# Optimization experiments

Hardware: AMD Instinct MI355X
Metric: run time of the kernel (lower is better)

The kernel has to match this reference:

```python
import jax, jax.numpy as jnp
import numpy as np

B, S, H = 1024, 512, 768
D1, D2 = 128, 1


def setup_inputs() -> dict:
    key = jax.random.key(0)
    k_feat, k_start, k_len, k_w1, k_w2 = jax.random.split(key, 5)
    features_extract = jax.random.normal(k_feat, (B, S, H), dtype=jnp.float32)
    start_token_idx = jax.random.randint(k_start, (B,), 1, 200, dtype=jnp.int64)
    span_len = jax.random.randint(k_len, (B,), 1, 65, dtype=jnp.int64)
    end_token_idx = start_token_idx + span_len  # guaranteed start < end <= 264 < S
    W1 = jax.random.normal(k_w1, (2 * H, D1), dtype=jnp.float32) * (1.0 / np.sqrt(2 * H))
    b1 = jnp.zeros((D1,), dtype=jnp.float32)
    W2 = jax.random.normal(k_w2, (D1, D2), dtype=jnp.float32) * (1.0 / np.sqrt(D1))
    b2 = jnp.zeros((D2,), dtype=jnp.float32)
    return {
        "features_extract": features_extract,
        "start_token_idx": start_token_idx,
        "end_token_idx": end_token_idx,
        "W1": W1, "b1": b1, "W2": W2, "b2": b2,
    }


def reference(features_extract, start_token_idx, end_token_idx, W1, b1, W2, b2):
    # CLS feature: token 0 of each example -> [B, 1, H]
    features_cls = features_extract[:, 0, :][:, None, :]

    # Ragged span mean-pool (vectorized replacement for the per-example loop):
    # mask[b, s] = start[b] <= s < end[b]
    pos = jnp.arange(features_extract.shape[1])  # [S]
    mask = (pos[None, :] >= start_token_idx[:, None]) & (pos[None, :] < end_token_idx[:, None])
    maskf = mask.astype(features_extract.dtype)  # [B, S]
    span_sum = jnp.einsum('bsh,bs->bh', features_extract, maskf)
    span_len = (end_token_idx - start_token_idx).astype(features_extract.dtype)  # >= 1
    features_crc = (span_sum / span_len[:, None])[:, None, :]  # [B, 1, H]

    # Concat + MLP head (dropout layers are identity in eval)
    features = jnp.concatenate([features_cls, features_crc], axis=2)  # [B, 1, 2H]
    h = jax.nn.relu(jnp.einsum('bid,dk->bik', features, W1) + b1)
    out = jax.nn.sigmoid(jnp.einsum('bik,ko->bio', h, W2) + b2)  # [B, 1, 1]
    return out
```

## Files before the change

kernel.cpp:

```cpp
#include <hip/hip_runtime.h>
#include <math.h>

constexpr int Bn = 1024;
constexpr int S  = 512;
constexpr int H  = 768;
constexpr int D1 = 128;
constexpr int HV = H / 4;
constexpr int NH = 512;


__global__ __launch_bounds__(256) void fused_pool_clshead(
    const float* __restrict__ feat, const int* __restrict__ start,
    const int* __restrict__ endp, float* __restrict__ gp,
    const float* __restrict__ W1, float* __restrict__ P) {
  __shared__ float g[4][384];
  __shared__ float part[2][4][D1];

  const int t = threadIdx.x;

  if (blockIdx.x < NH) {
    const int c = blockIdx.x & 1;
    const int e0 = (blockIdx.x >> 1) * 4;
    const int dglob0 = c * 384;

    for (int i = t; i < 384; i += 256) {
      const int e = i / 96;
      const int j = i % 96;
      float4 v = *reinterpret_cast<const float4*>(
          feat + (size_t)(e0 + e) * S * H + dglob0 + j * 4);
      reinterpret_cast<float4*>(&g[e][0])[j] = v;
    }
    __syncthreads();

    const int k = t & (D1 - 1);
    const int sub = t >> 7;
    const int gofs = sub * 192;
    const float* Wc = W1 + (size_t)(dglob0 + gofs) * D1 + k;

    float a0 = 0.f, a1 = 0.f, a2 = 0.f, a3 = 0.f;
    #pragma unroll 4
    for (int d = 0; d < 192; d += 4) {
      float w0 = Wc[(size_t)(d + 0) * D1];
      float w1 = Wc[(size_t)(d + 1) * D1];
      float w2 = Wc[(size_t)(d + 2) * D1];
      float w3 = Wc[(size_t)(d + 3) * D1];
      float4 g0 = *reinterpret_cast<const float4*>(&g[0][gofs + d]);
      float4 g1 = *reinterpret_cast<const float4*>(&g[1][gofs + d]);
      float4 g2 = *reinterpret_cast<const float4*>(&g[2][gofs + d]);
      float4 g3 = *reinterpret_cast<const float4*>(&g[3][gofs + d]);
      a0 += g0.x * w0 + g0.y * w1 + g0.z * w2 + g0.w * w3;
      a1 += g1.x * w0 + g1.y * w1 + g1.z * w2 + g1.w * w3;
      a2 += g2.x * w0 + g2.y * w1 + g2.z * w2 + g2.w * w3;
      a3 += g3.x * w0 + g3.y * w1 + g3.z * w2 + g3.w * w3;
    }
    part[sub][0][k] = a0;
    part[sub][1][k] = a1;
    part[sub][2][k] = a2;
    part[sub][3][k] = a3;
    __syncthreads();

    if (t < D1) {
      #pragma unroll
      for (int e = 0; e < 4; ++e) {
        P[((size_t)c * Bn + (e0 + e)) * D1 + t] = part[0][e][t] + part[1][e][t];
      }
    }
    return;
  }

  if (t >= 192) return;
  const int bb = blockIdx.x - NH;
  const int b = bb >> 1;
  const int p = bb & 1;
  const float4* base = reinterpret_cast<const float4*>(feat) + (size_t)b * (S * HV);

  const int s0 = start[b];
  const int s1 = endp[b];
  float4 a0{0,0,0,0}, a1{0,0,0,0}, a2{0,0,0,0}, a3{0,0,0,0};
  int s = s0 + p;
  for (; s + 6 < s1; s += 8) {
    float4 v0 = base[(size_t)(s    ) * HV + t];
    float4 v1 = base[(size_t)(s + 2) * HV + t];
    float4 v2 = base[(size_t)(s + 4) * HV + t];
    float4 v3 = base[(size_t)(s + 6) * HV + t];
    a0.x += v0.x; a0.y += v0.y; a0.z += v0.z; a0.w += v0.w;
    a1.x += v1.x; a1.y += v1.y; a1.z += v1.z; a1.w += v1.w;
    a2.x += v2.x; a2.y += v2.y; a2.z += v2.z; a2.w += v2.w;
    a3.x += v3.x; a3.y += v3.y; a3.z += v3.z; a3.w += v3.w;
  }
  for (; s < s1; s += 2) {
    float4 v = base[(size_t)s * HV + t];
    a0.x += v.x; a0.y += v.y; a0.z += v.z; a0.w += v.w;
  }
  const float inv = 1.0f / (float)(s1 - s0);
  float4 r;
  r.x = ((a0.x + a1.x) + (a2.x + a3.x)) * inv;
  r.y = ((a0.y + a1.y) + (a2.y + a3.y)) * inv;
  r.z = ((a0.z + a1.z) + (a2.z + a3.z)) * inv;
  r.w = ((a0.w + a1.w) + (a2.w + a3.w)) * inv;
  reinterpret_cast<float4*>(gp)[((size_t)p * Bn + b) * HV + t] = r;
}

__global__ __launch_bounds__(256) void crc_head_finalize(
    const float* __restrict__ gp, const float* __restrict__ W1,
    const float* __restrict__ P, const float* __restrict__ b1,
    const float* __restrict__ W2, const float* __restrict__ b2,
    float* __restrict__ out) {
  __shared__ float g[4][768];
  __shared__ float part[2][4][D1];

  const int t = threadIdx.x;
  const int e0 = blockIdx.x * 4;

  for (int i = t; i < 768; i += 256) {
    const int e = i / 192;
    const int j = i % 192;
    const float* b0 = gp + (size_t)(e0 + e) * H;
    float4 u0 = reinterpret_cast<const float4*>(b0)[j];
    float4 u1 = reinterpret_cast<const float4*>(b0 + (size_t)Bn * H)[j];
    float4 v;
    v.x = u0.x + u1.x; v.y = u0.y + u1.y;
    v.z = u0.z + u1.z; v.w = u0.w + u1.w;
    reinterpret_cast<float4*>(&g[e][0])[j] = v;
  }
  __syncthreads();

  const int k = t & (D1 - 1);
  const int sub = t >> 7;
  const int gofs = sub * 384;
  const float* Wc = W1 + (size_t)(H + gofs) * D1 + k;

  float a0 = 0.f, a1 = 0.f, a2 = 0.f, a3 = 0.f;
  #pragma unroll 4
  for (int d = 0; d < 384; d += 4) {
    float w0 = Wc[(size_t)(d + 0) * D1];
    float w1 = Wc[(size_t)(d + 1) * D1];
    float w2 = Wc[(size_t)(d + 2) * D1];
    float w3 = Wc[(size_t)(d + 3) * D1];
    float4 g0 = *reinterpret_cast<const float4*>(&g[0][gofs + d]);
    float4 g1 = *reinterpret_cast<const float4*>(&g[1][gofs + d]);
    float4 g2 = *reinterpret_cast<const float4*>(&g[2][gofs + d]);
    float4 g3 = *reinterpret_cast<const float4*>(&g[3][gofs + d]);
    a0 += g0.x * w0 + g0.y * w1 + g0.z * w2 + g0.w * w3;
    a1 += g1.x * w0 + g1.y * w1 + g1.z * w2 + g1.w * w3;
    a2 += g2.x * w0 + g2.y * w1 + g2.z * w2 + g2.w * w3;
    a3 += g3.x * w0 + g3.y * w1 + g3.z * w2 + g3.w * w3;
  }
  part[sub][0][k] = a0;
  part[sub][1][k] = a1;
  part[sub][2][k] = a2;
  part[sub][3][k] = a3;
  __syncthreads();

  {
    const int w = t >> 6, l = t & 63;
    const int e = e0 + w;
    const int k0 = l, k1 = l + 64;
    float h0 = b1[k0] + part[0][w][k0] + part[1][w][k0]
             + P[((size_t)0 * Bn + e) * D1 + k0]
             + P[((size_t)1 * Bn + e) * D1 + k0];
    float h1 = b1[k1] + part[0][w][k1] + part[1][w][k1]
             + P[((size_t)0 * Bn + e) * D1 + k1]
             + P[((size_t)1 * Bn + e) * D1 + k1];
    h0 = fmaxf(h0, 0.f); h1 = fmaxf(h1, 0.f);
    float v = h0 * W2[k0] + h1 * W2[k1];
    #pragma unroll
    for (int off = 32; off > 0; off >>= 1) v += __shfl_down(v, off);
    if (l == 0) out[e] = 1.0f / (1.0f + expf(-(v + b2[0])));
  }
}

extern "C" void kernel_launch(void* const* d_in, const int* in_sizes, int n_in,
                              void* d_out, int out_size, void* d_ws, size_t ws_size,
                              hipStream_t stream) {
  const float* feat = (const float*)d_in[0];
  const int* start  = (const int*)d_in[1];
  const int* endp   = (const int*)d_in[2];
  const float* W1   = (const float*)d_in[3];
  const float* b1   = (const float*)d_in[4];
  const float* W2   = (const float*)d_in[5];
  const float* b2   = (const float*)d_in[6];
  float* out = (float*)d_out;

  float* wsf = (float*)d_ws;
  float* gp  = wsf;
  float* P   = gp + (size_t)2 * Bn * H;

  hipLaunchKernelGGL(fused_pool_clshead, dim3(NH + Bn * 2), dim3(256), 0,
                     stream, feat, start, endp, gp, W1, P);
  hipLaunchKernelGGL(crc_head_finalize, dim3(Bn / 4), dim3(256), 0, stream,
                     gp, W1, P, b1, W2, b2, out);
}
```

Measured before the change: 36.93 us.

## Merge pool and head kernels into one launch with atomic flag dataflow

Result: slower. 143.5 us (+288.7%).

```diff
diff --git a/kernel.cpp b/kernel.cpp
--- a/kernel.cpp
+++ b/kernel.cpp
@@ -6,21 +6,78 @@
 constexpr int H  = 768;
 constexpr int D1 = 128;
 constexpr int HV = H / 4;
-constexpr int NH = 512;
-
-
-__global__ __launch_bounds__(256) void fused_pool_clshead(
+
+constexpr int NPOOL = Bn * 2;
+constexpr int NCLS  = 512;
+constexpr int NCRC  = 512;
+constexpr int NFIN  = Bn / 4;
+
+
+__device__ __forceinline__ void release_add(unsigned* f) {
+  __hip_atomic_fetch_add(f, 1u, __ATOMIC_RELEASE, __HIP_MEMORY_SCOPE_AGENT);
+}
+__device__ __forceinline__ void acquire_spin(const unsigned* f, unsigned need) {
+  while (__hip_atomic_load(f, __ATOMIC_ACQUIRE, __HIP_MEMORY_SCOPE_AGENT) < need) {
+    __builtin_amdgcn_s_sleep(8);
+  }
+}
+
+__global__ __launch_bounds__(256) void mega(
     const float* __restrict__ feat, const int* __restrict__ start,
-    const int* __restrict__ endp, float* __restrict__ gp,
-    const float* __restrict__ W1, float* __restrict__ P) {
+    const int* __restrict__ endp, const float* __restrict__ W1,
+    const float* __restrict__ b1, const float* __restrict__ W2,
+    const float* __restrict__ b2, unsigned* __restrict__ flag1,
+    unsigned* __restrict__ flag2, float* __restrict__ gp,
+    float* __restrict__ P, float* __restrict__ out) {
   __shared__ float g[4][384];
   __shared__ float part[2][4][D1];
 
   const int t = threadIdx.x;
-
-  if (blockIdx.x < NH) {
-    const int c = blockIdx.x & 1;
-    const int e0 = (blockIdx.x >> 1) * 4;
+  const unsigned bid = blockIdx.x;
+
+  if (bid < NPOOL) {
+    const int b = bid >> 1;
+    const int p = bid & 1;
+    const int eg = b >> 2;
+    if (t < 192) {
+      const float4* base =
+          reinterpret_cast<const float4*>(feat) + (size_t)b * (S * HV);
+      const int s0 = start[b];
+      const int s1 = endp[b];
+      float4 a0{0,0,0,0}, a1{0,0,0,0}, a2{0,0,0,0}, a3{0,0,0,0};
+      int s = s0 + p;
+      for (; s + 6 < s1; s += 8) {
+        float4 v0 = base[(size_t)(s    ) * HV + t];
+        float4 v1 = base[(size_t)(s + 2) * HV + t];
+        float4 v2 = base[(size_t)(s + 4) * HV + t];
+        float4 v3 = base[(size_t)(s + 6) * HV + t];
+        a0.x += v0.x; a0.y += v0.y; a0.z += v0.z; a0.w += v0.w;
+        a1.x += v1.x; a1.y += v1.y; a1.z += v1.z; a1.w += v1.w;
+        a2.x += v2.x; a2.y += v2.y; a2.z += v2.z; a2.w += v2.w;
+        a3.x += v3.x; a3.y += v3.y; a3.z += v3.z; a3.w += v3.w;
+      }
+      for (; s < s1; s += 2) {
+        float4 v = base[(size_t)s * HV + t];
+        a0.x += v.x; a0.y += v.y; a0.z += v.z; a0.w += v.w;
+      }
+      const float inv = 1.0f / (float)(s1 - s0);
+      float4 r;
+      r.x = ((a0.x + a1.x) + (a2.x + a3.x)) * inv;
+      r.y = ((a0.y + a1.y) + (a2.y + a3.y)) * inv;
+      r.z = ((a0.z + a1.z) + (a2.z + a3.z)) * inv;
+      r.w = ((a0.w + a1.w) + (a2.w + a3.w)) * inv;
+      reinterpret_cast<float4*>(gp)[((size_t)p * Bn + b) * HV + t] = r;
+    }
+    __syncthreads();
+    if (t == 0) release_add(&flag1[eg]);
+    return;
+  }
+
+  if (bid < NPOOL + NCLS) {
+    const int hb = bid - NPOOL;
+    const int c = hb & 1;
+    const int eg = hb >> 1;
+    const int e0 = eg * 4;
     const int dglob0 = c * 384;
 
     for (int i = t; i < 384; i += 256) {
@@ -65,103 +122,88 @@
         P[((size_t)c * Bn + (e0 + e)) * D1 + t] = part[0][e][t] + part[1][e][t];
       }
     }
+    __syncthreads();
+    if (t == 0) release_add(&flag2[eg]);
     return;
   }
 
-  if (t >= 192) return;
-  const int bb = blockIdx.x - NH;
-  const int b = bb >> 1;
-  const int p = bb & 1;
-  const float4* base = reinterpret_cast<const float4*>(feat) + (size_t)b * (S * HV);
-
-  const int s0 = start[b];
-  const int s1 = endp[b];
-  float4 a0{0,0,0,0}, a1{0,0,0,0}, a2{0,0,0,0}, a3{0,0,0,0};
-  int s = s0 + p;
-  for (; s + 6 < s1; s += 8) {
-    float4 v0 = base[(size_t)(s    ) * HV + t];
-    float4 v1 = base[(size_t)(s + 2) * HV + t];
-    float4 v2 = base[(size_t)(s + 4) * HV + t];
-    float4 v3 = base[(size_t)(s + 6) * HV + t];
-    a0.x += v0.x; a0.y += v0.y; a0.z += v0.z; a0.w += v0.w;
-    a1.x += v1.x; a1.y += v1.y; a1.z += v1.z; a1.w += v1.w;
-    a2.x += v2.x; a2.y += v2.y; a2.z += v2.z; a2.w += v2.w;
-    a3.x += v3.x; a3.y += v3.y; a3.z += v3.z; a3.w += v3.w;
-  }
-  for (; s < s1; s += 2) {
-    float4 v = base[(size_t)s * HV + t];
-    a0.x += v.x; a0.y += v.y; a0.z += v.z; a0.w += v.w;
-  }
-  const float inv = 1.0f / (float)(s1 - s0);
-  float4 r;
-  r.x = ((a0.x + a1.x) + (a2.x + a3.x)) * inv;
-  r.y = ((a0.y + a1.y) + (a2.y + a3.y)) * inv;
-  r.z = ((a0.z + a1.z) + (a2.z + a3.z)) * inv;
-  r.w = ((a0.w + a1.w) + (a2.w + a3.w)) * inv;
-  reinterpret_cast<float4*>(gp)[((size_t)p * Bn + b) * HV + t] = r;
-}
-
-__global__ __launch_bounds__(256) void crc_head_finalize(
-    const float* __restrict__ gp, const float* __restrict__ W1,
-    const float* __restrict__ P, const float* __restrict__ b1,
-    const float* __restrict__ W2, const float* __restrict__ b2,
-    float* __restrict__ out) {
-  __shared__ float g[4][768];
-  __shared__ float part[2][4][D1];
-
-  const int t = threadIdx.x;
-  const int e0 = blockIdx.x * 4;
-
-  for (int i = t; i < 768; i += 256) {
-    const int e = i / 192;
-    const int j = i % 192;
-    const float* b0 = gp + (size_t)(e0 + e) * H;
-    float4 u0 = reinterpret_cast<const float4*>(b0)[j];
-    float4 u1 = reinterpret_cast<const float4*>(b0 + (size_t)Bn * H)[j];
-    float4 v;
-    v.x = u0.x + u1.x; v.y = u0.y + u1.y;
-    v.z = u0.z + u1.z; v.w = u0.w + u1.w;
-    reinterpret_cast<float4*>(&g[e][0])[j] = v;
-  }
-  __syncthreads();
-
-  const int k = t & (D1 - 1);
-  const int sub = t >> 7;
-  const int gofs = sub * 384;
-  const float* Wc = W1 + (size_t)(H + gofs) * D1 + k;
-
-  float a0 = 0.f, a1 = 0.f, a2 = 0.f, a3 = 0.f;
-  #pragma unroll 4
-  for (int d = 0; d < 384; d += 4) {
-    float w0 = Wc[(size_t)(d + 0) * D1];
-    float w1 = Wc[(size_t)(d + 1) * D1];
-    float w2 = Wc[(size_t)(d + 2) * D1];
-    float w3 = Wc[(size_t)(d + 3) * D1];
-    float4 g0 = *reinterpret_cast<const float4*>(&g[0][gofs + d]);
-    float4 g1 = *reinterpret_cast<const float4*>(&g[1][gofs + d]);
-    float4 g2 = *reinterpret_cast<const float4*>(&g[2][gofs + d]);
-    float4 g3 = *reinterpret_cast<const float4*>(&g[3][gofs + d]);
-    a0 += g0.x * w0 + g0.y * w1 + g0.z * w2 + g0.w * w3;
-    a1 += g1.x * w0 + g1.y * w1 + g1.z * w2 + g1.w * w3;
-    a2 += g2.x * w0 + g2.y * w1 + g2.z * w2 + g2.w * w3;
-    a3 += g3.x * w0 + g3.y * w1 + g3.z * w2 + g3.w * w3;
-  }
-  part[sub][0][k] = a0;
-  part[sub][1][k] = a1;
-  part[sub][2][k] = a2;
-  part[sub][3][k] = a3;
-  __syncthreads();
+  if (bid < NPOOL + NCLS + NCRC) {
+    const int hb = bid - (NPOOL + NCLS);
+    const int c = 2 + (hb & 1);
+    const int eg = hb >> 1;
+    const int e0 = eg * 4;
+    const int dglob0 = c * 384;
+    const int dd0 = dglob0 - H;
+
+    if (t == 0) acquire_spin(&flag1[eg], 8u);
+    __syncthreads();
+
+    for (int i = t; i < 384; i += 256) {
+      const int e = i / 96;
+      const int j = i % 96;
+      const float* b0 = gp + (size_t)(e0 + e) * H + dd0;
+      float4 u0 = reinterpret_cast<const float4*>(b0)[j];
+      float4 u1 = reinterpret_cast<const float4*>(b0 + (size_t)Bn * H)[j];
+      float4 v;
+      v.x = u0.x + u1.x; v.y = u0.y + u1.y;
+      v.z = u0.z + u1.z; v.w = u0.w + u1.w;
+      reinterpret_cast<float4*>(&g[e][0])[j] = v;
+    }
+    __syncthreads();
+
+    const int k = t & (D1 - 1);
+    const int sub = t >> 7;
+    const int gofs = sub * 192;
+    const float* Wc = W1 + (size_t)(dglob0 + gofs) * D1 + k;
+
+    float a0 = 0.f, a1 = 0.f, a2 = 0.f, a3 = 0.f;
+    #pragma unroll 4
+    for (int d = 0; d < 192; d += 4) {
+      float w0 = Wc[(size_t)(d + 0) * D1];
+      float w1 = Wc[(size_t)(d + 1) * D1];
+      float w2 = Wc[(size_t)(d + 2) * D1];
+      float w3 = Wc[(size_t)(d + 3) * D1];
+      float4 g0 = *reinterpret_cast<const float4*>(&g[0][gofs + d]);
+      float4 g1 = *reinterpret_cast<const float4*>(&g[1][gofs + d]);
+      float4 g2 = *reinterpret_cast<const float4*>(&g[2][gofs + d]);
+      float4 g3 = *reinterpret_cast<const float4*>(&g[3][gofs + d]);
+      a0 += g0.x * w0 + g0.y * w1 + g0.z * w2 + g0.w * w3;
+      a1 += g1.x * w0 + g1.y * w1 + g1.z * w2 + g1.w * w3;
+      a2 += g2.x * w0 + g2.y * w1 + g2.z * w2 + g2.w * w3;
+      a3 += g3.x * w0 + g3.y * w1 + g3.z * w2 + g3.w * w3;
+    }
+    part[sub][0][k] = a0;
+    part[sub][1][k] = a1;
+    part[sub][2][k] = a2;
+    part[sub][3][k] = a3;
+    __syncthreads();
+
+    if (t < D1) {
+      #pragma unroll
+      for (int e = 0; e < 4; ++e) {
+        P[((size_t)c * Bn + (e0 + e)) * D1 + t] = part[0][e][t] + part[1][e][t];
+      }
+    }
+    __syncthreads();
+    if (t == 0) release_add(&flag2[eg]);
+    return;
+  }
 
   {
+    const int eg = bid - (NPOOL + NCLS + NCRC);
+    const int e0 = eg * 4;
+    if (t == 0) acquire_spin(&flag2[eg], 4u);
+    __syncthreads();
+
     const int w = t >> 6, l = t & 63;
     const int e = e0 + w;
     const int k0 = l, k1 = l + 64;
-    float h0 = b1[k0] + part[0][w][k0] + part[1][w][k0]
-             + P[((size_t)0 * Bn + e) * D1 + k0]
-             + P[((size_t)1 * Bn + e) * D1 + k0];
-    float h1 = b1[k1] + part[0][w][k1] + part[1][w][k1]
-             + P[((size_t)0 * Bn + e) * D1 + k1]
-             + P[((size_t)1 * Bn + e) * D1 + k1];
+    float h0 = b1[k0], h1 = b1[k1];
+    #pragma unroll
+    for (int c = 0; c < 4; ++c) {
+      h0 += P[((size_t)c * Bn + e) * D1 + k0];
+      h1 += P[((size_t)c * Bn + e) * D1 + k1];
+    }
     h0 = fmaxf(h0, 0.f); h1 = fmaxf(h1, 0.f);
     float v = h0 * W2[k0] + h1 * W2[k1];
     #pragma unroll
@@ -182,12 +224,13 @@
   const float* b2   = (const float*)d_in[6];
   float* out = (float*)d_out;
 
-  float* wsf = (float*)d_ws;
-  float* gp  = wsf;
-  float* P   = gp + (size_t)2 * Bn * H;
-
-  hipLaunchKernelGGL(fused_pool_clshead, dim3(NH + Bn * 2), dim3(256), 0,
-                     stream, feat, start, endp, gp, W1, P);
-  hipLaunchKernelGGL(crc_head_finalize, dim3(Bn / 4), dim3(256), 0, stream,
-                     gp, W1, P, b1, W2, b2, out);
-}
+  unsigned* flag1 = (unsigned*)d_ws;
+  unsigned* flag2 = flag1 + 256;
+  float* gp = (float*)((char*)d_ws + 4096);
+  float* P  = gp + (size_t)2 * Bn * H;
+
+  hipMemsetAsync(d_ws, 0, 4096, stream);
+  hipLaunchKernelGGL(mega, dim3(NPOOL + NCLS + NCRC + NFIN), dim3(256), 0,
+                     stream, feat, start, endp, W1, b1, W2, b2,
+                     flag1, flag2, gp, P, out);
+}
```

## Split CRC head matmul across four column chunks and add separate finalize kernel

Applied to the files above, without the earlier changes.

Result: faster. 33.96 us (-8.0%).

```diff
diff --git a/kernel.cpp b/kernel.cpp
--- a/kernel.cpp
+++ b/kernel.cpp
@@ -101,21 +101,21 @@
   reinterpret_cast<float4*>(gp)[((size_t)p * Bn + b) * HV + t] = r;
 }
 
-__global__ __launch_bounds__(256) void crc_head_finalize(
+__global__ __launch_bounds__(256) void crc_head(
     const float* __restrict__ gp, const float* __restrict__ W1,
-    const float* __restrict__ P, const float* __restrict__ b1,
-    const float* __restrict__ W2, const float* __restrict__ b2,
-    float* __restrict__ out) {
-  __shared__ float g[4][768];
+    float* __restrict__ P) {
+  __shared__ float g[4][192];
   __shared__ float part[2][4][D1];
 
   const int t = threadIdx.x;
-  const int e0 = blockIdx.x * 4;
-
-  for (int i = t; i < 768; i += 256) {
-    const int e = i / 192;
-    const int j = i % 192;
-    const float* b0 = gp + (size_t)(e0 + e) * H;
+  const int cc = blockIdx.x & 3;
+  const int e0 = (blockIdx.x >> 2) * 4;
+  const int dd0 = cc * 192;
+
+  for (int i = t; i < 192; i += 256) {
+    const int e = i / 48;
+    const int j = i % 48;
+    const float* b0 = gp + (size_t)(e0 + e) * H + dd0;
     float4 u0 = reinterpret_cast<const float4*>(b0)[j];
     float4 u1 = reinterpret_cast<const float4*>(b0 + (size_t)Bn * H)[j];
     float4 v;
@@ -127,12 +127,12 @@
 
   const int k = t & (D1 - 1);
   const int sub = t >> 7;
-  const int gofs = sub * 384;
-  const float* Wc = W1 + (size_t)(H + gofs) * D1 + k;
+  const int gofs = sub * 96;
+  const float* Wc = W1 + (size_t)(H + dd0 + gofs) * D1 + k;
 
   float a0 = 0.f, a1 = 0.f, a2 = 0.f, a3 = 0.f;
   #pragma unroll 4
-  for (int d = 0; d < 384; d += 4) {
+  for (int d = 0; d < 96; d += 4) {
     float w0 = Wc[(size_t)(d + 0) * D1];
     float w1 = Wc[(size_t)(d + 1) * D1];
     float w2 = Wc[(size_t)(d + 2) * D1];
@@ -152,22 +152,34 @@
   part[sub][3][k] = a3;
   __syncthreads();
 
-  {
-    const int w = t >> 6, l = t & 63;
-    const int e = e0 + w;
-    const int k0 = l, k1 = l + 64;
-    float h0 = b1[k0] + part[0][w][k0] + part[1][w][k0]
-             + P[((size_t)0 * Bn + e) * D1 + k0]
-             + P[((size_t)1 * Bn + e) * D1 + k0];
-    float h1 = b1[k1] + part[0][w][k1] + part[1][w][k1]
-             + P[((size_t)0 * Bn + e) * D1 + k1]
-             + P[((size_t)1 * Bn + e) * D1 + k1];
-    h0 = fmaxf(h0, 0.f); h1 = fmaxf(h1, 0.f);
-    float v = h0 * W2[k0] + h1 * W2[k1];
+  if (t < D1) {
     #pragma unroll
-    for (int off = 32; off > 0; off >>= 1) v += __shfl_down(v, off);
-    if (l == 0) out[e] = 1.0f / (1.0f + expf(-(v + b2[0])));
-  }
+    for (int e = 0; e < 4; ++e) {
+      P[((size_t)(2 + cc) * Bn + (e0 + e)) * D1 + t] =
+          part[0][e][t] + part[1][e][t];
+    }
+  }
+}
+
+__global__ __launch_bounds__(256) void finalize(
+    const float* __restrict__ P, const float* __restrict__ b1,
+    const float* __restrict__ W2, const float* __restrict__ b2,
+    float* __restrict__ out) {
+  const int t = threadIdx.x;
+  const int w = t >> 6, l = t & 63;
+  const int e = blockIdx.x * 4 + w;
+  const int k0 = l, k1 = l + 64;
+  float h0 = b1[k0], h1 = b1[k1];
+  #pragma unroll
+  for (int c = 0; c < 6; ++c) {
+    h0 += P[((size_t)c * Bn + e) * D1 + k0];
+    h1 += P[((size_t)c * Bn + e) * D1 + k1];
+  }
+  h0 = fmaxf(h0, 0.f); h1 = fmaxf(h1, 0.f);
+  float v = h0 * W2[k0] + h1 * W2[k1];
+  #pragma unroll
+  for (int off = 32; off > 0; off >>= 1) v += __shfl_down(v, off);
+  if (l == 0) out[e] = 1.0f / (1.0f + expf(-(v + b2[0])));
 }
 
 extern "C" void kernel_launch(void* const* d_in, const int* in_sizes, int n_in,
@@ -188,6 +200,7 @@
 
   hipLaunchKernelGGL(fused_pool_clshead, dim3(NH + Bn * 2), dim3(256), 0,
                      stream, feat, start, endp, gp, W1, P);
-  hipLaunchKernelGGL(crc_head_finalize, dim3(Bn / 4), dim3(256), 0, stream,
-                     gp, W1, P, b1, W2, b2, out);
-}
+  hipLaunchKernelGGL(crc_head, dim3(Bn), dim3(256), 0, stream, gp, W1, P);
+  hipLaunchKernelGGL(finalize, dim3(Bn / 4), dim3(256), 0, stream,
+                     P, b1, W2, b2, out);
+}
```
